# Performance work log

Measured on AMD Instinct MI355X. Metric: run time of the kernel, lower is better.

The kernel has to match this reference:

```python
import jax, jax.numpy as jnp
import numpy as np

D = 1024   # visual_dim
N = 64     # num_phrases(1) * topN(64)
DEG = 16   # edges per subject row (incl. one guaranteed via a permutation)
E = N * DEG
T = 2      # cfg.MODEL.RELATION.VISUAL_GRAPH_PASSING_TIME


def _graph():
    rng = np.random.default_rng(0)
    perm = rng.permutation(N)
    mask = np.zeros((N, N), bool)
    for i in range(N):
        mask[i, perm[i]] = True  # permutation guarantees every column is covered
        pool = np.delete(np.arange(N), perm[i])
        mask[i, rng.choice(pool, DEG - 1, replace=False)] = True
    hdim, wdim = np.nonzero(mask)  # row-major, exactly E entries
    conn = np.full((N, N), -1, np.int32)
    conn[hdim, wdim] = np.arange(hdim.shape[0])
    edge_idx = hdim * N + wdim  # original: hdim*topN + wdim (topN == N since num_phrases == 1)
    return conn, edge_idx.astype(np.int32)


def setup_inputs():
    conn, edge_idx = _graph()
    key = jax.random.key(0)
    ks = jax.random.split(key, 16)
    p = lambda k, shp: jax.random.normal(k, shp, jnp.float32) * 0.02
    return {
        'visual_feat': jax.random.normal(ks[0], (N, D), jnp.float32),
        'rel_visual_feat': jax.random.normal(ks[1], (E, D), jnp.float32),
        'conn_map': jnp.asarray(conn),
        'topN_boxes_ids': jnp.arange(N, dtype=jnp.int32)[None, :],  # only shape is used
        'edge_idx': jnp.asarray(edge_idx),
        'W_sub': p(ks[2], (D, D)),
        'W_obj': p(ks[3], (D, D)),
        'W_r2s': p(ks[4], (D, D)),
        'W_r2o': p(ks[5], (D, D)),
        'W_joint': p(ks[6], (D, 4 * D)),
        'W_ctx': p(ks[7], (D, 3 * D)),
        'W_rel_update': p(ks[8], (D, 3 * D)),
        'W_rel_joint': p(ks[9], (D, 4 * D)),
        'W_rel_ctx': p(ks[10], (D, 2 * D)),
        'W_node': p(ks[11], (D, 2 * D)),
        'b_node': jnp.zeros((D,), jnp.float32),
        'W_factor': p(ks[12], (D, 2 * D)),
    }


def _forward(visual_feat, rel_visual_feat, conn_map, edge_idx,
             W_sub, W_obj, W_r2s, W_r2o, W_joint, W_ctx, W_rel_update,
             W_rel_joint, W_rel_ctx, W_node, b_node, W_factor):
    n, d = visual_feat.shape
    scale = jnp.asarray(d, visual_feat.dtype) ** 0.5
    connected = conn_map >= 0
    # scatter edge features into the dense [N, N, D] grid
    rel_temp = (jnp.zeros((n * n, d), visual_feat.dtype)
                .at[edge_idx].set(rel_visual_feat)
                .reshape(n, n, d))
    rel_ctx = rel_temp
    vctx = visual_feat
    for _ in range(T):
        # joint node embedding  [N, D]
        vj = jnp.concatenate([visual_feat, vctx, visual_feat * vctx, vctx - visual_feat], 1) @ W_joint.T
        # joint edge embedding  [N, N, D] (1x1 conv == per-position linear)
        rj = jnp.einsum('ijd,od->ijo',
                        jnp.concatenate([rel_temp, rel_ctx, rel_temp * rel_ctx, rel_temp - rel_ctx], 2),
                        W_rel_joint)
        # node -> edge: cat(sub_tile, obj_tile, rj) @ W_rel_update, done without tiling
        Ws, Wo, Wr = W_rel_update[:, :d], W_rel_update[:, d:2 * d], W_rel_update[:, 2 * d:]
        rel_j = (vj @ Ws.T)[:, None, :] + (vj @ Wo.T)[None, :, :] + jnp.einsum('ijd,od->ijo', rj, Wr)
        # edge -> node attention scores (elementwise product of 1x1-conv outputs, summed over channels)
        s_sbj = jnp.einsum('id,ijd->ij', vj @ W_sub.T, jnp.einsum('ijd,od->ijo', rel_j, W_r2s)) / scale
        s_obj = jnp.einsum('jd,ijd->ij', vj @ W_obj.T, jnp.einsum('ijd,od->ijo', rel_j, W_r2o)) / scale
        w_sbj = jax.nn.softmax(jnp.where(connected, s_sbj, -jnp.inf), axis=1)
        w_obj = jax.nn.softmax(jnp.where(connected, s_obj, -jnp.inf), axis=0)
        ctx = jnp.concatenate([jnp.einsum('ijd,ij->id', rel_j, w_sbj),
                               jnp.einsum('ijd,ij->jd', rel_j, w_obj)], 1)
        vctx = jnp.concatenate([vctx, ctx], 1) @ W_ctx.T
        rel_ctx = jnp.einsum('ijd,od->ijo', jnp.concatenate([rel_ctx, rel_j], 2), W_rel_ctx)
    # gather back the valid edges and produce outputs
    rel_out = jnp.concatenate([rel_visual_feat, rel_ctx.reshape(-1, d)[edge_idx]], 1) @ W_factor.T
    v_out = jnp.concatenate([visual_feat, vctx], 1) @ W_node.T + b_node
    deg = connected.sum(1) + connected.sum(0)
    v_out = jnp.where((deg == 0)[:, None], visual_feat, v_out)  # isolated nodes pass through
    return rel_out, v_out


def reference(visual_feat, rel_visual_feat, conn_map, topN_boxes_ids, edge_idx,
              W_sub, W_obj, W_r2s, W_r2o, W_joint, W_ctx, W_rel_update,
              W_rel_joint, W_rel_ctx, W_node, b_node, W_factor):
    del topN_boxes_ids  # only its shape is used in the original
    return _forward(visual_feat, rel_visual_feat, conn_map, edge_idx,
                    W_sub, W_obj, W_r2s, W_r2o, W_joint, W_ctx, W_rel_update,
                    W_rel_joint, W_rel_ctx, W_node, b_node, W_factor)
```

## Files before the change

kernel.cpp:

```cpp
#include <hip/hip_runtime.h>

static constexpr int kN = 64;
static constexpr int kD = 1024;
static constexpr int kE = 1024;
static constexpr int kT = 2;

typedef short  bf16x8 __attribute__((ext_vector_type(8)));
typedef float  f32x4  __attribute__((ext_vector_type(4)));
typedef unsigned short us8 __attribute__((ext_vector_type(8)));
typedef unsigned short us4 __attribute__((ext_vector_type(4)));

__device__ __forceinline__ unsigned short f2b(float f) {
    unsigned int u = __builtin_bit_cast(unsigned int, f);
    u += 0x7FFFu + ((u >> 16) & 1u);
    return (unsigned short)(u >> 16);
}
__device__ __forceinline__ float b2f(unsigned short u) {
    unsigned int x = ((unsigned int)u) << 16;
    return __builtin_bit_cast(float, x);
}
__device__ __forceinline__ bf16x8 cvt8(float4 a, float4 b) {
    us8 o;
    o[0] = f2b(a.x); o[1] = f2b(a.y); o[2] = f2b(a.z); o[3] = f2b(a.w);
    o[4] = f2b(b.x); o[5] = f2b(b.y); o[6] = f2b(b.z); o[7] = f2b(b.w);
    return __builtin_bit_cast(bf16x8, o);
}

struct ASrc { const unsigned short* s0; const unsigned short* s1; const unsigned short* s2; int mode; };

__device__ __forceinline__ bf16x8 loadA8(const ASrc& s, int row, int kg) {
    const int seg = kg >> 10, k = kg & 1023;
    const size_t ro = (size_t)row * 1024 + k;
    if (s.mode == 1) {
        const unsigned short* p = (seg == 0) ? s.s0 : (seg == 1 ? s.s1 : s.s2);
        return *(const bf16x8*)(p + ro);
    }
    const bf16x8 a = *(const bf16x8*)(s.s0 + ro);
    if (seg == 0) return a;
    const bf16x8 b = *(const bf16x8*)(s.s1 + ro);
    const us8 ua = __builtin_bit_cast(us8, a), ub = __builtin_bit_cast(us8, b);
    us8 o;
#pragma unroll
    for (int q = 0; q < 8; ++q) o[q] = f2b(b2f(ua[q]) * b2f(ub[q]));
    return __builtin_bit_cast(bf16x8, o);
}

struct GJob { ASrc a; const unsigned short* W; int ldw; void* P; int M; int K; int KS; int pbf; };
struct GJobs { GJob j[5]; int t0[6]; int nj; };

__global__ __launch_bounds__(256)
void k_gemm(GJobs G)
{
    __shared__ unsigned short lds[16896];
    const int flat = blockIdx.x;
    int ji = 0;
    while (ji + 1 < G.nj && flat >= G.t0[ji + 1]) ++ji;
    const GJob J = G.j[ji];
    const int local = flat - G.t0[ji];
    const int tid = threadIdx.x, lane = tid & 63, wid = tid >> 6;
    const int l15 = lane & 15, l4 = lane >> 4;
    const int sr = tid >> 3, sc8 = tid & 7;
    const int wc8 = (sc8 ^ (sr & 7)) * 8;

    if (J.M >= 128) {
        const int rowTiles = J.M >> 7;
        const int rt = local % rowTiles;
        const int rest = local / rowTiles;
        const int ct = rest & 7, z = rest >> 3;
        const int rowBase = rt * 128, colBase = ct * 128;
        const int kchunk = J.K / J.KS, kbeg = z * kchunk, kend = kbeg + kchunk;
        const int wr = wid >> 1, wc = wid & 1;

        f32x4 acc[4][4] = {};
        bf16x8 ra[4], rb[4];
        auto stage = [&](int kt) {
#pragma unroll
            for (int h = 0; h < 4; ++h) {
                ra[h] = loadA8(J.a, rowBase + sr + 32 * h, kt + sc8 * 8);
                rb[h] = *(const bf16x8*)(J.W + (size_t)(colBase + sr + 32 * h) * J.ldw + kt + sc8 * 8);
            }
        };

        stage(kbeg);
        for (int kt = kbeg; kt < kend; kt += 64) {
            __syncthreads();
#pragma unroll
            for (int h = 0; h < 4; ++h) {
                *(bf16x8*)&lds[(sr + 32 * h) * 64 + wc8] = ra[h];
                *(bf16x8*)&lds[8192 + (sr + 32 * h) * 64 + wc8] = rb[h];
            }
            __syncthreads();
            if (kt + 64 < kend) stage(kt + 64);
#pragma unroll
            for (int kk = 0; kk < 2; ++kk) {
                bf16x8 af[4], bv[4];
#pragma unroll
                for (int m = 0; m < 4; ++m) {
                    const int ar = wr * 64 + m * 16 + l15;
                    af[m] = *(const bf16x8*)&lds[ar * 64 + (((kk << 2) | l4) ^ (ar & 7)) * 8];
                }
#pragma unroll
                for (int n = 0; n < 4; ++n) {
                    const int br = wc * 64 + n * 16 + l15;
                    bv[n] = *(const bf16x8*)&lds[8192 + br * 64 + (((kk << 2) | l4) ^ (br & 7)) * 8];
                }
#pragma unroll
                for (int m = 0; m < 4; ++m)
#pragma unroll
                    for (int n = 0; n < 4; ++n)
                        acc[m][n] = __builtin_amdgcn_mfma_f32_16x16x32_bf16(af[m], bv[n], acc[m][n], 0, 0, 0);
            }
        }

        __syncthreads();
#pragma unroll
        for (int m = 0; m < 4; ++m)
#pragma unroll
            for (int n = 0; n < 4; ++n)
#pragma unroll
                for (int r = 0; r < 4; ++r)
                    lds[(wr * 64 + m * 16 + l4 * 4 + r) * 132 + wc * 64 + n * 16 + l15] =
                        f2b(acc[m][n][r]);
        __syncthreads();
        unsigned short* Pb = (unsigned short*)J.P + (size_t)z * J.M * 1024;
#pragma unroll
        for (int c = tid; c < 2048; c += 256) {
            const int row = c >> 4, ch = c & 15;
            *(bf16x8*)(Pb + (size_t)(rowBase + row) * 1024 + colBase + ch * 8) =
                *(const bf16x8*)&lds[row * 132 + ch * 8];
        }
    } else {
        const int ct = local & 7, z = local >> 3;
        const int colBase = ct * 128;
        const int kchunk = J.K / J.KS, kbeg = z * kchunk, kend = kbeg + kchunk;
        const int wr = wid >> 1, wc = wid & 1;

        bf16x8 ra[2], rb[4];
        auto stage = [&](int kt) {
#pragma unroll
            for (int h = 0; h < 2; ++h)
                ra[h] = loadA8(J.a, sr + 32 * h, kt + sc8 * 8);
#pragma unroll
            for (int h = 0; h < 4; ++h)
                rb[h] = *(const bf16x8*)(J.W + (size_t)(colBase + sr + 32 * h) * J.ldw + kt + sc8 * 8);
        };

        f32x4 acc[2][4] = {};
        stage(kbeg);
        for (int kt = kbeg; kt < kend; kt += 64) {
            __syncthreads();
#pragma unroll
            for (int h = 0; h < 2; ++h)
                *(bf16x8*)&lds[(sr + 32 * h) * 64 + wc8] = ra[h];
#pragma unroll
            for (int h = 0; h < 4; ++h)
                *(bf16x8*)&lds[4096 + (sr + 32 * h) * 64 + wc8] = rb[h];
            __syncthreads();
            if (kt + 64 < kend) stage(kt + 64);
#pragma unroll
            for (int kk = 0; kk < 2; ++kk) {
                const int c8 = kk * 4 + l4;
                bf16x8 af[2], bv[4];
#pragma unroll
                for (int m = 0; m < 2; ++m) {
                    const int ar = wr * 32 + m * 16 + l15;
                    af[m] = *(const bf16x8*)&lds[ar * 64 + (c8 ^ (ar & 7)) * 8];
                }
#pragma unroll
                for (int n = 0; n < 4; ++n) {
                    const int br = wc * 64 + n * 16 + l15;
                    bv[n] = *(const bf16x8*)&lds[4096 + br * 64 + (c8 ^ (br & 7)) * 8];
                }
#pragma unroll
                for (int m = 0; m < 2; ++m)
#pragma unroll
                    for (int n = 0; n < 4; ++n)
                        acc[m][n] = __builtin_amdgcn_mfma_f32_16x16x32_bf16(af[m], bv[n], acc[m][n], 0, 0, 0);
            }
        }
        float* base = (float*)J.P + (size_t)z * J.M * 1024;
#pragma unroll
        for (int m = 0; m < 2; ++m) {
            const int row = wr * 32 + m * 16 + l4 * 4;
#pragma unroll
            for (int n = 0; n < 4; ++n) {
                const int col = colBase + wc * 64 + n * 16 + l15;
#pragma unroll
                for (int r = 0; r < 4; ++r)
                    base[(size_t)(row + r) * 1024 + col] = acc[m][n][r];
            }
        }
    }
}

struct RJob { const void* P; int MO8; int KS; int pbf; float* Cf; unsigned short* Cb;
              const unsigned short* addb; const float* bias; int gather; };
struct RJobs { RJob j[6]; int t0[7]; int nj; const int* eidx; const float* gP; int gKS; };

__global__ void k_reduce(RJobs R)
{
    const int flat = blockIdx.x;
    int ji = 0;
    while (ji + 1 < R.nj && flat >= R.t0[ji + 1]) ++ji;
    const RJob J = R.j[ji];
    const int i8 = (flat - R.t0[ji]) * 256 + threadIdx.x;
    if (i8 >= J.MO8) return;
    float s[8] = {0.f, 0.f, 0.f, 0.f, 0.f, 0.f, 0.f, 0.f};
    if (J.pbf) {
        const unsigned short* P = (const unsigned short*)J.P;
        for (int z = 0; z < J.KS; ++z) {
            const us8 v = *(const us8*)(P + (size_t)z * J.MO8 * 8 + (size_t)i8 * 8);
#pragma unroll
            for (int q = 0; q < 8; ++q) s[q] += b2f(v[q]);
        }
    } else {
        const float* P = (const float*)J.P;
        for (int z = 0; z < J.KS; ++z) {
            const float* p = P + (size_t)z * J.MO8 * 8 + (size_t)i8 * 8;
            const float4 v0 = *(const float4*)p;
            const float4 v1 = *(const float4*)(p + 4);
            s[0] += v0.x; s[1] += v0.y; s[2] += v0.z; s[3] += v0.w;
            s[4] += v1.x; s[5] += v1.y; s[6] += v1.z; s[7] += v1.w;
        }
    }
    if (J.addb) {
        const us8 v = *(const us8*)(J.addb + (size_t)i8 * 8);
#pragma unroll
        for (int q = 0; q < 8; ++q) s[q] += b2f(v[q]);
    }
    if (J.gather) {
        const int e = i8 >> 7, c8 = i8 & 127;
        const int idx = R.eidx[e];
        const float* as_ = R.gP + (size_t)(idx >> 6) * 1024 + c8 * 8;
        const float* ao_ = R.gP + 131072 + (size_t)(idx & 63) * 1024 + c8 * 8;
        for (int z = 0; z < R.gKS; ++z) {
#pragma unroll
            for (int q = 0; q < 8; ++q)
                s[q] += as_[(size_t)z * 65536 + q] + ao_[(size_t)z * 65536 + q];
        }
    }
    if (J.bias) {
        const int c8 = i8 & 127;
#pragma unroll
        for (int q = 0; q < 8; ++q) s[q] += J.bias[c8 * 8 + q];
    }
    if (J.Cf) {
        *(float4*)(J.Cf + (size_t)i8 * 8)     = make_float4(s[0], s[1], s[2], s[3]);
        *(float4*)(J.Cf + (size_t)i8 * 8 + 4) = make_float4(s[4], s[5], s[6], s[7]);
    }
    if (J.Cb) {
        us8 o;
#pragma unroll
        for (int q = 0; q < 8; ++q) o[q] = f2b(s[q]);
        *(us8*)(J.Cb + (size_t)i8 * 8) = o;
    }
}

struct ConvBatch { const float* s[7]; unsigned short* d[7]; int beg8[7]; int total8; };
__global__ void k_f2b_batch(ConvBatch cb)
{
    int i = blockIdx.x * blockDim.x + threadIdx.x;
    if (i >= cb.total8) return;
    int k = 0;
    while (k < 6 && i >= cb.beg8[k + 1]) ++k;
    const int j = i - cb.beg8[k];
    const float4 v0 = reinterpret_cast<const float4*>(cb.s[k])[2 * j];
    const float4 v1 = reinterpret_cast<const float4*>(cb.s[k])[2 * j + 1];
    const bf16x8 o = cvt8(v0, v1);
    *(bf16x8*)(cb.d[k] + (size_t)j * 8) = o;
}

struct T4 { const float* s[4]; unsigned short* d[4]; };
__global__ __launch_bounds__(256)
void k_transpose(T4 t4)
{
    __shared__ float tile[64][65];
    const float* __restrict__ src = t4.s[blockIdx.z];
    unsigned short* __restrict__ dst = t4.d[blockIdx.z];
    const int bx = blockIdx.x * 64, by = blockIdx.y * 64;
    const int c = threadIdx.x & 63, r0 = threadIdx.x >> 6;
#pragma unroll
    for (int h = 0; h < 16; ++h) {
        const int r = r0 * 16 + h;
        tile[r][c] = src[(size_t)(by + r) * 1024 + bx + c];
    }
    __syncthreads();
#pragma unroll
    for (int h = 0; h < 16; ++h) {
        const int kk = r0 * 16 + h;
        dst[(size_t)(bx + kk) * 1024 + by + c] = f2b(tile[c][kk]);
    }
}

__global__ __launch_bounds__(256)
void k_buildW(const float* __restrict__ Wrel, const float* __restrict__ Wjnt,
              unsigned short* __restrict__ WrtRel, unsigned short* __restrict__ WeffRel,
              unsigned short* __restrict__ UrtVj, unsigned short* __restrict__ UeffVj)
{
    const int idx = blockIdx.x * 256 + threadIdx.x;
    const int o = idx >> 8, j = (idx & 255) * 4;
    const float* W = blockIdx.z ? Wjnt : Wrel;
    const float sgn = blockIdx.z ? -1.f : 1.f;
    unsigned short* rt = blockIdx.z ? UrtVj : WrtRel;
    unsigned short* ef = blockIdx.z ? UeffVj : WeffRel;
    const float4 w1 = *(const float4*)(W + (size_t)o * 4096 + j);
    const float4 w2 = *(const float4*)(W + (size_t)o * 4096 + 1024 + j);
    const float4 w3 = *(const float4*)(W + (size_t)o * 4096 + 2048 + j);
    const float4 w4 = *(const float4*)(W + (size_t)o * 4096 + 3072 + j);
    us4 t;
    t.x = f2b(w1.x + sgn * w4.x); t.y = f2b(w1.y + sgn * w4.y);
    t.z = f2b(w1.z + sgn * w4.z); t.w = f2b(w1.w + sgn * w4.w);
    *(us4*)(rt + (size_t)o * 1024 + j) = t;
    t.x = f2b(w2.x - sgn * w4.x); t.y = f2b(w2.y - sgn * w4.y);
    t.z = f2b(w2.z - sgn * w4.z); t.w = f2b(w2.w - sgn * w4.w);
    *(us4*)(ef + (size_t)o * 2048 + j) = t;
    t.x = f2b(w3.x); t.y = f2b(w3.y); t.z = f2b(w3.z); t.w = f2b(w3.w);
    *(us4*)(ef + (size_t)o * 2048 + 1024 + j) = t;
}

__global__ __launch_bounds__(256)
void k_sctx(const float* __restrict__ relj, const float* __restrict__ qws,
            const float* __restrict__ qwo, const int* __restrict__ conn,
            unsigned short* __restrict__ ctx1b, unsigned short* __restrict__ ctx2b)
{
    const int bid = blockIdx.x, t = threadIdx.x;
    const float4* relj4 = reinterpret_cast<const float4*>(relj);
    __shared__ float sl[64];
    __shared__ int el[64];
    float4 acc = make_float4(0.f, 0.f, 0.f, 0.f);

    if (bid < 64) {
        const int i = bid;
        {
            const int g = t >> 4, l = t & 15;
            const size_t e4 = (size_t)(i * 16 + g) * 256;
            const float4* q4 = reinterpret_cast<const float4*>(qws) + (size_t)i * 256;
            float v = 0.f;
#pragma unroll
            for (int q = 0; q < 16; ++q) {
                const float4 r = relj4[e4 + l + q * 16];
                const float4 a = q4[l + q * 16];
                v += a.x * r.x + a.y * r.y + a.z * r.z + a.w * r.w;
            }
            v += __shfl_xor(v, 1, 16);
            v += __shfl_xor(v, 2, 16);
            v += __shfl_xor(v, 4, 16);
            v += __shfl_xor(v, 8, 16);
            if (l == 0) sl[g] = v * 0.03125f;
        }
        __syncthreads();
        float sv[16];
        float m = -1e30f;
#pragma unroll
        for (int q = 0; q < 16; ++q) { sv[q] = sl[q]; m = fmaxf(m, sv[q]); }
        float sum = 0.f;
#pragma unroll
        for (int q = 0; q < 16; ++q) { sv[q] = expf(sv[q] - m); sum += sv[q]; }
        const float inv = 1.f / sum;
#pragma unroll
        for (int q = 0; q < 16; ++q) {
            const float w = sv[q] * inv;
            const float4 v = relj4[(size_t)(i * 16 + q) * 256 + t];
            acc.x += w * v.x; acc.y += w * v.y; acc.z += w * v.z; acc.w += w * v.w;
        }
        us4 o; o.x = f2b(acc.x); o.y = f2b(acc.y); o.z = f2b(acc.z); o.w = f2b(acc.w);
        *(us4*)(ctx1b + (size_t)i * 1024 + t * 4) = o;
    } else {
        const int j = bid - 64;
        {
            const int i = t >> 2, sub = t & 3;
            const int e = conn[i * kN + j];
            if (sub == 0) el[i] = e;
            float v = 0.f;
            if (e >= 0) {
                const size_t e4 = (size_t)e * 256;
                const float4* q4 = reinterpret_cast<const float4*>(qwo) + (size_t)j * 256;
#pragma unroll
                for (int q = 0; q < 64; ++q) {
                    const float4 r = relj4[e4 + sub + q * 4];
                    const float4 a = q4[sub + q * 4];
                    v += a.x * r.x + a.y * r.y + a.z * r.z + a.w * r.w;
                }
            }
            v += __shfl_xor(v, 1, 4);
            v += __shfl_xor(v, 2, 4);
            if (sub == 0) sl[i] = (e >= 0) ? v * 0.03125f : -1e30f;
        }
        __syncthreads();
        float m = -1e30f;
        for (int i = 0; i < 64; ++i) m = fmaxf(m, sl[i]);
        float sum = 0.f;
        float ex[64];
        for (int i = 0; i < 64; ++i) {
            ex[i] = (el[i] >= 0) ? expf(sl[i] - m) : 0.f;
            sum += ex[i];
        }
        const float inv = 1.f / sum;
        for (int i = 0; i < 64; ++i) {
            const int e = el[i];
            if (e >= 0) {
                const float w = ex[i] * inv;
                const float4 v = relj4[(size_t)e * 256 + t];
                acc.x += w * v.x; acc.y += w * v.y; acc.z += w * v.z; acc.w += w * v.w;
            }
        }
        us4 o; o.x = f2b(acc.x); o.y = f2b(acc.y); o.z = f2b(acc.z); o.w = f2b(acc.w);
        *(us4*)(ctx2b + (size_t)j * 1024 + t * 4) = o;
    }
}

extern "C" void kernel_launch(void* const* d_in, const int* in_sizes, int n_in,
                              void* d_out, int out_size, void* d_ws, size_t ws_size,
                              hipStream_t stream)
{
    const float* visual   = (const float*)d_in[0];
    const float* relvis   = (const float*)d_in[1];
    const int*   conn     = (const int*)d_in[2];
    const int*   edge_idx = (const int*)d_in[4];
    const float* W_sub    = (const float*)d_in[5];
    const float* W_obj    = (const float*)d_in[6];
    const float* W_r2s    = (const float*)d_in[7];
    const float* W_r2o    = (const float*)d_in[8];
    const float* W_joint  = (const float*)d_in[9];
    const float* W_ctx    = (const float*)d_in[10];
    const float* W_relu   = (const float*)d_in[11];
    const float* W_relj   = (const float*)d_in[12];
    const float* W_relc   = (const float*)d_in[13];
    const float* W_node   = (const float*)d_in[14];
    const float* b_node   = (const float*)d_in[15];
    const float* W_factor = (const float*)d_in[16];
    (void)in_sizes; (void)n_in; (void)out_size; (void)ws_size;

    float* ws = (float*)d_ws;
    size_t off = 0;
    auto allocF = [&](size_t n) { float* p = ws + off; off += n; return p; };
    auto allocU = [&](size_t n) { return (unsigned short*)allocF((n + 1) / 2); };

    float* partF = allocF((size_t)1024 * 1024);
    unsigned short* partB = allocU((size_t)16 * 1024 * 1024);
    float* asqw  = allocF((size_t)4 * 64 * 1024);
    float* relj  = allocF((size_t)kE * kD);
    unsigned short* relvis_b = allocU((size_t)kE * kD);
    unsigned short* visual_b = allocU((size_t)kN * kD);
    unsigned short* vj_b   = allocU((size_t)kN * kD);
    unsigned short* rj_b   = allocU((size_t)kE * kD);
    unsigned short* relj_b = allocU((size_t)kE * kD);
    unsigned short* rc_bA  = allocU((size_t)kE * kD);
    unsigned short* rc_bB  = allocU((size_t)kE * kD);
    unsigned short* vctx_bA = allocU((size_t)kN * kD);
    unsigned short* vctx_bB = allocU((size_t)kN * kD);
    unsigned short* ctx1_b = allocU((size_t)kN * kD);
    unsigned short* ctx2_b = allocU((size_t)kN * kD);
    unsigned short* R0_b = allocU((size_t)kE * kD);
    unsigned short* G0_b = allocU((size_t)kN * kD);
    unsigned short* Wb_ctx    = allocU((size_t)kD * 3 * kD);
    unsigned short* Wb_relu   = allocU((size_t)kD * 3 * kD);
    unsigned short* Wb_relc   = allocU((size_t)kD * 2 * kD);
    unsigned short* Wb_node   = allocU((size_t)kD * 2 * kD);
    unsigned short* Wb_factor = allocU((size_t)kD * 2 * kD);
    unsigned short* WsubT = allocU((size_t)kD * kD);
    unsigned short* WobjT = allocU((size_t)kD * kD);
    unsigned short* Wr2sT = allocU((size_t)kD * kD);
    unsigned short* Wr2oT = allocU((size_t)kD * kD);
    unsigned short* Wc_s  = allocU((size_t)kD * kD);
    unsigned short* Wc_o  = allocU((size_t)kD * kD);
    unsigned short* WrtRel  = allocU((size_t)kD * kD);
    unsigned short* WeffRel = allocU((size_t)kD * 2 * kD);
    unsigned short* UrtVj   = allocU((size_t)kD * kD);
    unsigned short* UeffVj  = allocU((size_t)kD * 2 * kD);

    auto seg1 = [](const unsigned short* a) {
        ASrc s; s.s0 = a; s.s1 = nullptr; s.s2 = nullptr; s.mode = 1; return s;
    };
    auto seg2 = [](const unsigned short* a, const unsigned short* b) {
        ASrc s; s.s0 = a; s.s1 = b; s.s2 = nullptr; s.mode = 1; return s;
    };
    auto seg3 = [](const unsigned short* a, const unsigned short* b, const unsigned short* c) {
        ASrc s; s.s0 = a; s.s1 = b; s.s2 = c; s.mode = 1; return s;
    };
    auto prodA = [](const unsigned short* c, const unsigned short* x) {
        ASrc s; s.s0 = c; s.s1 = x; s.s2 = nullptr; s.mode = 2; return s;
    };

    GJobs G; RJobs R;
    int gn = 0, gt = 0, rn = 0, rtt = 0;
    auto gAdd = [&](ASrc a, const unsigned short* W, int ldw, void* P, int M, int K, int KS, int pbf) {
        G.j[gn].a = a; G.j[gn].W = W; G.j[gn].ldw = ldw; G.j[gn].P = P;
        G.j[gn].M = M; G.j[gn].K = K; G.j[gn].KS = KS; G.j[gn].pbf = pbf;
        G.t0[gn] = gt;
        gt += (M >= 128) ? KS * (M >> 7) * 8 : KS * 8;
        ++gn;
    };
    auto gLaunch = [&]() {
        G.nj = gn; G.t0[gn] = gt;
        hipLaunchKernelGGL(k_gemm, dim3(gt), dim3(256), 0, stream, G);
        gn = 0; gt = 0;
    };
    auto rAdd = [&](const void* P, int MO8, int KS, int pbf, float* Cf, unsigned short* Cb,
                    const unsigned short* addb, const float* bias, int gather) {
        R.j[rn].P = P; R.j[rn].MO8 = MO8; R.j[rn].KS = KS; R.j[rn].pbf = pbf;
        R.j[rn].Cf = Cf; R.j[rn].Cb = Cb; R.j[rn].addb = addb; R.j[rn].bias = bias;
        R.j[rn].gather = gather;
        R.t0[rn] = rtt; rtt += (MO8 + 255) / 256; ++rn;
    };
    auto rLaunch = [&](const int* eidx, const float* gP, int gKS) {
        R.nj = rn; R.t0[rn] = rtt; R.eidx = eidx; R.gP = gP; R.gKS = gKS;
        hipLaunchKernelGGL(k_reduce, dim3(rtt), dim3(256), 0, stream, R);
        rn = 0; rtt = 0;
    };

    {
        ConvBatch cb;
        const float* srcs[7] = {W_ctx, W_relu, W_relc, W_node, W_factor, relvis, visual};
        unsigned short* dsts[7] = {Wb_ctx, Wb_relu, Wb_relc, Wb_node, Wb_factor, relvis_b, visual_b};
        const int nel[7] = {3 * 1024 * 1024, 3 * 1024 * 1024, 2 * 1024 * 1024,
                            2 * 1024 * 1024, 2 * 1024 * 1024, 1024 * 1024, 64 * 1024};
        int cum = 0;
        for (int k = 0; k < 7; ++k) { cb.s[k] = srcs[k]; cb.d[k] = dsts[k]; cb.beg8[k] = cum; cum += nel[k] / 8; }
        cb.total8 = cum;
        hipLaunchKernelGGL(k_f2b_batch, dim3((cum + 255) / 256), dim3(256), 0, stream, cb);
    }
    {
        T4 t4;
        t4.s[0] = W_sub; t4.d[0] = WsubT;
        t4.s[1] = W_obj; t4.d[1] = WobjT;
        t4.s[2] = W_r2s; t4.d[2] = Wr2sT;
        t4.s[3] = W_r2o; t4.d[3] = Wr2oT;
        hipLaunchKernelGGL(k_transpose, dim3(16, 16, 4), dim3(256), 0, stream, t4);
    }
    hipLaunchKernelGGL(k_buildW, dim3(1024, 1, 2), dim3(256), 0, stream,
                       W_relj, W_joint, WrtRel, WeffRel, UrtVj, UeffVj);

    const size_t PB1 = (size_t)4 * 1024 * 1024;
    gAdd(seg1(Wr2sT), WsubT, 1024, partB, 1024, 1024, 4, 1);
    gAdd(seg1(Wr2oT), WobjT, 1024, partB + PB1, 1024, 1024, 4, 1);
    gAdd(seg1(relvis_b), WrtRel, 1024, partB + 2 * PB1, 1024, 1024, 4, 1);
    gAdd(seg1(visual_b), UrtVj, 1024, partF, 64, 1024, 4, 0);
    gLaunch();
    rAdd(partB, 131072, 4, 1, nullptr, Wc_s, nullptr, nullptr, 0);
    rAdd(partB + PB1, 131072, 4, 1, nullptr, Wc_o, nullptr, nullptr, 0);
    rAdd(partB + 2 * PB1, 131072, 4, 1, nullptr, R0_b, nullptr, nullptr, 0);
    rAdd(partF, 8192, 4, 0, nullptr, G0_b, nullptr, nullptr, 0);
    rLaunch(nullptr, nullptr, 0);

    for (int t = 0; t < kT; ++t) {
        const unsigned short* vcur  = (t == 0) ? visual_b : vctx_bA;
        unsigned short*       vnext = (t == 0) ? vctx_bA : vctx_bB;
        const unsigned short* rccur = (t == 0) ? relvis_b : rc_bA;
        unsigned short*       rcnext = (t == 0) ? rc_bA : rc_bB;

        gAdd(prodA(vcur, visual_b), UeffVj, 2048, partF, 64, 2048, 8, 0);
        gAdd(prodA(rccur, relvis_b), WeffRel, 2048, partB, 1024, 2048, 8, 1);
        gLaunch();
        rAdd(partF, 8192, 8, 0, nullptr, vj_b, G0_b, nullptr, 0);
        rAdd(partB, 131072, 8, 1, nullptr, rj_b, R0_b, nullptr, 0);
        rLaunch(nullptr, nullptr, 0);

        gAdd(seg1(vj_b), Wb_relu,        3072, partF,          64, 1024, 2, 0);
        gAdd(seg1(vj_b), Wb_relu + 1024, 3072, partF + 131072, 64, 1024, 2, 0);
        gAdd(seg1(vj_b), Wc_s,           1024, partF + 262144, 64, 1024, 2, 0);
        gAdd(seg1(vj_b), Wc_o,           1024, partF + 393216, 64, 1024, 2, 0);
        gAdd(seg1(rj_b), Wb_relu + 2048, 3072, partB,        1024, 1024, 4, 1);
        gLaunch();
        rAdd(partF,          8192, 2, 0, asqw,          nullptr, nullptr, nullptr, 0);
        rAdd(partF + 131072, 8192, 2, 0, asqw + 65536,  nullptr, nullptr, nullptr, 0);
        rAdd(partF + 262144, 8192, 2, 0, asqw + 131072, nullptr, nullptr, nullptr, 0);
        rAdd(partF + 393216, 8192, 2, 0, asqw + 196608, nullptr, nullptr, nullptr, 0);
        rAdd(partB, 131072, 4, 1, relj, relj_b, nullptr, nullptr, 1);
        rLaunch(edge_idx, partF, 2);

        hipLaunchKernelGGL(k_sctx, dim3(128), dim3(256), 0, stream,
                           relj, asqw + 131072, asqw + 196608, conn, ctx1_b, ctx2_b);

        gAdd(seg3(vcur, ctx1_b, ctx2_b), Wb_ctx, 3072, partF, 64, 3072, 8, 0);
        gAdd(seg2(rccur, relj_b), Wb_relc, 2048, partB, 1024, 2048, 8, 1);
        gLaunch();
        rAdd(partF, 8192, 8, 0, nullptr, vnext, nullptr, nullptr, 0);
        rAdd(partB, 131072, 8, 1, nullptr, rcnext, nullptr, nullptr, 0);
        rLaunch(nullptr, nullptr, 0);
    }

    float* rel_out = (float*)d_out;
    float* v_out   = (float*)d_out + (size_t)kE * kD;
    gAdd(seg2(relvis_b, rc_bB), Wb_factor, 2048, partB, 1024, 2048, 4, 1);
    gAdd(seg2(visual_b, vctx_bB), Wb_node, 2048, partF, 64, 2048, 8, 0);
    gLaunch();
    rAdd(partB, 131072, 4, 1, rel_out, nullptr, nullptr, nullptr, 0);
    rAdd(partF, 8192, 8, 0, v_out, nullptr, nullptr, b_node, 0);
    rLaunch(nullptr, nullptr, 0);
}
```

Measured before the change: 230.0 us.

## Fuse split-K reduction into GEMM via last-block atomic counter epilogue

```diff
diff --git a/kernel.cpp b/kernel.cpp
--- a/kernel.cpp
+++ b/kernel.cpp
@@ -45,143 +45,102 @@
     return __builtin_bit_cast(bf16x8, o);
 }
 
-struct GJob { ASrc a; const unsigned short* W; int ldw; void* P; int M; int K; int KS; int pbf; };
-struct GJobs { GJob j[5]; int t0[6]; int nj; };
+struct GEpi { float* Cf; unsigned short* Cb; const unsigned short* addb;
+              const float* bias; int tail; int cbase; };
+struct GJob { ASrc a; const unsigned short* W; int ldw; void* P; int M; int K; int KS; int pbf;
+              GEpi e; };
+struct GJobs { GJob j[6]; int t0[7]; int nj; int* cnt; };
 
 __global__ __launch_bounds__(256)
 void k_gemm(GJobs G)
 {
-    __shared__ unsigned short lds[16896];
+    __shared__ unsigned short lds[12288];
+    __shared__ int lastFlag;
     const int flat = blockIdx.x;
     int ji = 0;
     while (ji + 1 < G.nj && flat >= G.t0[ji + 1]) ++ji;
     const GJob J = G.j[ji];
     const int local = flat - G.t0[ji];
+    const int rowTiles = J.M >> 6;
+    const int rt = local & (rowTiles - 1);
+    const int rest = local / rowTiles;
+    const int ct = rest & 7, z = rest >> 3;
+    const int rowBase = rt * 64, colBase = ct * 128;
+    const int kchunk = J.K / J.KS, kbeg = z * kchunk, kend = kbeg + kchunk;
+
     const int tid = threadIdx.x, lane = tid & 63, wid = tid >> 6;
     const int l15 = lane & 15, l4 = lane >> 4;
     const int sr = tid >> 3, sc8 = tid & 7;
     const int wc8 = (sc8 ^ (sr & 7)) * 8;
-
-    if (J.M >= 128) {
-        const int rowTiles = J.M >> 7;
-        const int rt = local % rowTiles;
-        const int rest = local / rowTiles;
-        const int ct = rest & 7, z = rest >> 3;
-        const int rowBase = rt * 128, colBase = ct * 128;
-        const int kchunk = J.K / J.KS, kbeg = z * kchunk, kend = kbeg + kchunk;
-        const int wr = wid >> 1, wc = wid & 1;
-
-        f32x4 acc[4][4] = {};
-        bf16x8 ra[4], rb[4];
-        auto stage = [&](int kt) {
-#pragma unroll
-            for (int h = 0; h < 4; ++h) {
-                ra[h] = loadA8(J.a, rowBase + sr + 32 * h, kt + sc8 * 8);
-                rb[h] = *(const bf16x8*)(J.W + (size_t)(colBase + sr + 32 * h) * J.ldw + kt + sc8 * 8);
-            }
-        };
-
-        stage(kbeg);
-        for (int kt = kbeg; kt < kend; kt += 64) {
-            __syncthreads();
-#pragma unroll
-            for (int h = 0; h < 4; ++h) {
-                *(bf16x8*)&lds[(sr + 32 * h) * 64 + wc8] = ra[h];
-                *(bf16x8*)&lds[8192 + (sr + 32 * h) * 64 + wc8] = rb[h];
-            }
-            __syncthreads();
-            if (kt + 64 < kend) stage(kt + 64);
-#pragma unroll
-            for (int kk = 0; kk < 2; ++kk) {
-                bf16x8 af[4], bv[4];
-#pragma unroll
-                for (int m = 0; m < 4; ++m) {
-                    const int ar = wr * 64 + m * 16 + l15;
-                    af[m] = *(const bf16x8*)&lds[ar * 64 + (((kk << 2) | l4) ^ (ar & 7)) * 8];
-                }
-#pragma unroll
-                for (int n = 0; n < 4; ++n) {
-                    const int br = wc * 64 + n * 16 + l15;
-                    bv[n] = *(const bf16x8*)&lds[8192 + br * 64 + (((kk << 2) | l4) ^ (br & 7)) * 8];
-                }
-#pragma unroll
-                for (int m = 0; m < 4; ++m)
-#pragma unroll
-                    for (int n = 0; n < 4; ++n)
-                        acc[m][n] = __builtin_amdgcn_mfma_f32_16x16x32_bf16(af[m], bv[n], acc[m][n], 0, 0, 0);
-            }
-        }
-
+    const int wr = wid >> 1, wc = wid & 1;
+
+    bf16x8 ra[2], rb[4];
+    auto stage = [&](int kt) {
+#pragma unroll
+        for (int h = 0; h < 2; ++h)
+            ra[h] = loadA8(J.a, rowBase + sr + 32 * h, kt + sc8 * 8);
+#pragma unroll
+        for (int h = 0; h < 4; ++h)
+            rb[h] = *(const bf16x8*)(J.W + (size_t)(colBase + sr + 32 * h) * J.ldw + kt + sc8 * 8);
+    };
+
+    f32x4 acc[2][4] = {};
+    stage(kbeg);
+    for (int kt = kbeg; kt < kend; kt += 64) {
         __syncthreads();
 #pragma unroll
-        for (int m = 0; m < 4; ++m)
+        for (int h = 0; h < 2; ++h)
+            *(bf16x8*)&lds[(sr + 32 * h) * 64 + wc8] = ra[h];
+#pragma unroll
+        for (int h = 0; h < 4; ++h)
+            *(bf16x8*)&lds[4096 + (sr + 32 * h) * 64 + wc8] = rb[h];
+        __syncthreads();
+        if (kt + 64 < kend) stage(kt + 64);
+#pragma unroll
+        for (int kk = 0; kk < 2; ++kk) {
+            const int c8 = kk * 4 + l4;
+            bf16x8 af[2], bv[4];
+#pragma unroll
+            for (int m = 0; m < 2; ++m) {
+                const int ar = wr * 32 + m * 16 + l15;
+                af[m] = *(const bf16x8*)&lds[ar * 64 + (c8 ^ (ar & 7)) * 8];
+            }
+#pragma unroll
+            for (int n = 0; n < 4; ++n) {
+                const int br = wc * 64 + n * 16 + l15;
+                bv[n] = *(const bf16x8*)&lds[4096 + br * 64 + (c8 ^ (br & 7)) * 8];
+            }
+#pragma unroll
+            for (int m = 0; m < 2; ++m)
+#pragma unroll
+                for (int n = 0; n < 4; ++n)
+                    acc[m][n] = __builtin_amdgcn_mfma_f32_16x16x32_bf16(af[m], bv[n], acc[m][n], 0, 0, 0);
+        }
+    }
+
+    if (J.pbf) {
+        __syncthreads();
+#pragma unroll
+        for (int m = 0; m < 2; ++m)
 #pragma unroll
             for (int n = 0; n < 4; ++n)
 #pragma unroll
                 for (int r = 0; r < 4; ++r)
-                    lds[(wr * 64 + m * 16 + l4 * 4 + r) * 132 + wc * 64 + n * 16 + l15] =
+                    lds[(wr * 32 + m * 16 + l4 * 4 + r) * 132 + wc * 64 + n * 16 + l15] =
                         f2b(acc[m][n][r]);
         __syncthreads();
         unsigned short* Pb = (unsigned short*)J.P + (size_t)z * J.M * 1024;
 #pragma unroll
-        for (int c = tid; c < 2048; c += 256) {
+        for (int c = tid; c < 1024; c += 256) {
             const int row = c >> 4, ch = c & 15;
             *(bf16x8*)(Pb + (size_t)(rowBase + row) * 1024 + colBase + ch * 8) =
                 *(const bf16x8*)&lds[row * 132 + ch * 8];
         }
     } else {
-        const int ct = local & 7, z = local >> 3;
-        const int colBase = ct * 128;
-        const int kchunk = J.K / J.KS, kbeg = z * kchunk, kend = kbeg + kchunk;
-        const int wr = wid >> 1, wc = wid & 1;
-
-        bf16x8 ra[2], rb[4];
-        auto stage = [&](int kt) {
-#pragma unroll
-            for (int h = 0; h < 2; ++h)
-                ra[h] = loadA8(J.a, sr + 32 * h, kt + sc8 * 8);
-#pragma unroll
-            for (int h = 0; h < 4; ++h)
-                rb[h] = *(const bf16x8*)(J.W + (size_t)(colBase + sr + 32 * h) * J.ldw + kt + sc8 * 8);
-        };
-
-        f32x4 acc[2][4] = {};
-        stage(kbeg);
-        for (int kt = kbeg; kt < kend; kt += 64) {
-            __syncthreads();
-#pragma unroll
-            for (int h = 0; h < 2; ++h)
-                *(bf16x8*)&lds[(sr + 32 * h) * 64 + wc8] = ra[h];
-#pragma unroll
-            for (int h = 0; h < 4; ++h)
-                *(bf16x8*)&lds[4096 + (sr + 32 * h) * 64 + wc8] = rb[h];
-            __syncthreads();
-            if (kt + 64 < kend) stage(kt + 64);
-#pragma unroll
-            for (int kk = 0; kk < 2; ++kk) {
-                const int c8 = kk * 4 + l4;
-                bf16x8 af[2], bv[4];
-#pragma unroll
-                for (int m = 0; m < 2; ++m) {
-                    const int ar = wr * 32 + m * 16 + l15;
-                    af[m] = *(const bf16x8*)&lds[ar * 64 + (c8 ^ (ar & 7)) * 8];
-                }
-#pragma unroll
-                for (int n = 0; n < 4; ++n) {
-                    const int br = wc * 64 + n * 16 + l15;
-                    bv[n] = *(const bf16x8*)&lds[4096 + br * 64 + (c8 ^ (br & 7)) * 8];
-                }
-#pragma unroll
-                for (int m = 0; m < 2; ++m)
-#pragma unroll
-                    for (int n = 0; n < 4; ++n)
-                        acc[m][n] = __builtin_amdgcn_mfma_f32_16x16x32_bf16(af[m], bv[n], acc[m][n], 0, 0, 0);
-            }
-        }
         float* base = (float*)J.P + (size_t)z * J.M * 1024;
 #pragma unroll
         for (int m = 0; m < 2; ++m) {
-            const int row = wr * 32 + m * 16 + l4 * 4;
+            const int row = rowBase + wr * 32 + m * 16 + l4 * 4;
 #pragma unroll
             for (int n = 0; n < 4; ++n) {
                 const int col = colBase + wc * 64 + n * 16 + l15;
@@ -191,69 +150,87 @@
             }
         }
     }
-}
-
-struct RJob { const void* P; int MO8; int KS; int pbf; float* Cf; unsigned short* Cb;
-              const unsigned short* addb; const float* bias; int gather; };
-struct RJobs { RJob j[6]; int t0[7]; int nj; const int* eidx; const float* gP; int gKS; };
-
-__global__ void k_reduce(RJobs R)
-{
-    const int flat = blockIdx.x;
-    int ji = 0;
-    while (ji + 1 < R.nj && flat >= R.t0[ji + 1]) ++ji;
-    const RJob J = R.j[ji];
-    const int i8 = (flat - R.t0[ji]) * 256 + threadIdx.x;
-    if (i8 >= J.MO8) return;
+
+    if (!J.e.tail) return;
+    __syncthreads();
+    if (tid == 0) {
+        __threadfence();
+        lastFlag = (atomicAdd(&G.cnt[J.e.cbase + rt * 8 + ct], 1) == J.KS - 1);
+    }
+    __syncthreads();
+    if (!lastFlag) return;
+    __threadfence();
+
+    const int rr = tid >> 2, c0 = (tid & 3) * 32;
+    const int grow = rowBase + rr;
+#pragma unroll
+    for (int g = 0; g < 4; ++g) {
+        const int col = colBase + c0 + g * 8;
+        const size_t oidx = (size_t)grow * 1024 + col;
+        float s[8] = {0.f, 0.f, 0.f, 0.f, 0.f, 0.f, 0.f, 0.f};
+        if (J.pbf) {
+            const unsigned short* Pb = (const unsigned short*)J.P;
+            for (int zz = 0; zz < J.KS; ++zz) {
+                const us8 v = *(const us8*)(Pb + (size_t)zz * J.M * 1024 + oidx);
+#pragma unroll
+                for (int q = 0; q < 8; ++q) s[q] += b2f(v[q]);
+            }
+        } else {
+            const float* Pf = (const float*)J.P;
+            for (int zz = 0; zz < J.KS; ++zz) {
+                const float* p = Pf + (size_t)zz * J.M * 1024 + oidx;
+                const float4 v0 = *(const float4*)p;
+                const float4 v1 = *(const float4*)(p + 4);
+                s[0] += v0.x; s[1] += v0.y; s[2] += v0.z; s[3] += v0.w;
+                s[4] += v1.x; s[5] += v1.y; s[6] += v1.z; s[7] += v1.w;
+            }
+        }
+        if (J.e.addb) {
+            const us8 v = *(const us8*)(J.e.addb + oidx);
+#pragma unroll
+            for (int q = 0; q < 8; ++q) s[q] += b2f(v[q]);
+        }
+        if (J.e.bias) {
+#pragma unroll
+            for (int q = 0; q < 8; ++q) s[q] += J.e.bias[col + q];
+        }
+        if (J.e.Cf) {
+            *(float4*)(J.e.Cf + oidx)     = make_float4(s[0], s[1], s[2], s[3]);
+            *(float4*)(J.e.Cf + oidx + 4) = make_float4(s[4], s[5], s[6], s[7]);
+        }
+        if (J.e.Cb) {
+            us8 o;
+#pragma unroll
+            for (int q = 0; q < 8; ++q) o[q] = f2b(s[q]);
+            *(us8*)(J.e.Cb + oidx) = o;
+        }
+    }
+}
+
+__global__ void k_relj(const unsigned short* __restrict__ P, int KS,
+                       const float* __restrict__ a_s, const float* __restrict__ a_o,
+                       const int* __restrict__ eidx,
+                       float* __restrict__ Cf, unsigned short* __restrict__ Cb)
+{
+    const int i8 = blockIdx.x * 256 + threadIdx.x;
     float s[8] = {0.f, 0.f, 0.f, 0.f, 0.f, 0.f, 0.f, 0.f};
-    if (J.pbf) {
-        const unsigned short* P = (const unsigned short*)J.P;
-        for (int z = 0; z < J.KS; ++z) {
-            const us8 v = *(const us8*)(P + (size_t)z * J.MO8 * 8 + (size_t)i8 * 8);
-#pragma unroll
-            for (int q = 0; q < 8; ++q) s[q] += b2f(v[q]);
-        }
-    } else {
-        const float* P = (const float*)J.P;
-        for (int z = 0; z < J.KS; ++z) {
-            const float* p = P + (size_t)z * J.MO8 * 8 + (size_t)i8 * 8;
-            const float4 v0 = *(const float4*)p;
-            const float4 v1 = *(const float4*)(p + 4);
-            s[0] += v0.x; s[1] += v0.y; s[2] += v0.z; s[3] += v0.w;
-            s[4] += v1.x; s[5] += v1.y; s[6] += v1.z; s[7] += v1.w;
-        }
-    }
-    if (J.addb) {
-        const us8 v = *(const us8*)(J.addb + (size_t)i8 * 8);
+    for (int z = 0; z < KS; ++z) {
+        const us8 v = *(const us8*)(P + (size_t)z * 1048576 + (size_t)i8 * 8);
 #pragma unroll
         for (int q = 0; q < 8; ++q) s[q] += b2f(v[q]);
     }
-    if (J.gather) {
-        const int e = i8 >> 7, c8 = i8 & 127;
-        const int idx = R.eidx[e];
-        const float* as_ = R.gP + (size_t)(idx >> 6) * 1024 + c8 * 8;
-        const float* ao_ = R.gP + 131072 + (size_t)(idx & 63) * 1024 + c8 * 8;
-        for (int z = 0; z < R.gKS; ++z) {
-#pragma unroll
-            for (int q = 0; q < 8; ++q)
-                s[q] += as_[(size_t)z * 65536 + q] + ao_[(size_t)z * 65536 + q];
-        }
-    }
-    if (J.bias) {
-        const int c8 = i8 & 127;
-#pragma unroll
-        for (int q = 0; q < 8; ++q) s[q] += J.bias[c8 * 8 + q];
-    }
-    if (J.Cf) {
-        *(float4*)(J.Cf + (size_t)i8 * 8)     = make_float4(s[0], s[1], s[2], s[3]);
-        *(float4*)(J.Cf + (size_t)i8 * 8 + 4) = make_float4(s[4], s[5], s[6], s[7]);
-    }
-    if (J.Cb) {
-        us8 o;
-#pragma unroll
-        for (int q = 0; q < 8; ++q) o[q] = f2b(s[q]);
-        *(us8*)(J.Cb + (size_t)i8 * 8) = o;
-    }
+    const int e = i8 >> 7, c8 = i8 & 127;
+    const int idx = eidx[e];
+    const float* as_ = a_s + (size_t)(idx >> 6) * 1024 + c8 * 8;
+    const float* ao_ = a_o + (size_t)(idx & 63) * 1024 + c8 * 8;
+#pragma unroll
+    for (int q = 0; q < 8; ++q) s[q] += as_[q] + ao_[q];
+    *(float4*)(Cf + (size_t)i8 * 8)     = make_float4(s[0], s[1], s[2], s[3]);
+    *(float4*)(Cf + (size_t)i8 * 8 + 4) = make_float4(s[4], s[5], s[6], s[7]);
+    us8 o;
+#pragma unroll
+    for (int q = 0; q < 8; ++q) o[q] = f2b(s[q]);
+    *(us8*)(Cb + (size_t)i8 * 8) = o;
 }
 
 struct ConvBatch { const float* s[7]; unsigned short* d[7]; int beg8[7]; int total8; };
@@ -431,8 +408,9 @@
     const float* W_factor = (const float*)d_in[16];
     (void)in_sizes; (void)n_in; (void)out_size; (void)ws_size;
 
+    int* cnt = (int*)d_ws;
     float* ws = (float*)d_ws;
-    size_t off = 0;
+    size_t off = 2048;
     auto allocF = [&](size_t n) { float* p = ws + off; off += n; return p; };
     auto allocU = [&](size_t n) { return (unsigned short*)allocF((n + 1) / 2); };
 
@@ -481,33 +459,33 @@
     auto prodA = [](const unsigned short* c, const unsigned short* x) {
         ASrc s; s.s0 = c; s.s1 = x; s.s2 = nullptr; s.mode = 2; return s;
     };
-
-    GJobs G; RJobs R;
-    int gn = 0, gt = 0, rn = 0, rtt = 0;
-    auto gAdd = [&](ASrc a, const unsigned short* W, int ldw, void* P, int M, int K, int KS, int pbf) {
+    auto epi = [](float* Cf, unsigned short* Cb, const unsigned short* addb,
+                  const float* bias) {
+        GEpi e; e.Cf = Cf; e.Cb = Cb; e.addb = addb; e.bias = bias; e.tail = 1; e.cbase = 0;
+        return e;
+    };
+    auto noepi = []() {
+        GEpi e; e.Cf = nullptr; e.Cb = nullptr; e.addb = nullptr; e.bias = nullptr;
+        e.tail = 0; e.cbase = 0; return e;
+    };
+
+    GJobs G;
+    G.cnt = cnt;
+    int gn = 0, gt = 0, cOff = 0;
+    auto gAdd = [&](ASrc a, const unsigned short* W, int ldw, void* P, int M, int K, int KS,
+                    int pbf, GEpi e) {
+        if (e.tail) { e.cbase = cOff; cOff += (M >> 6) * 8; }
         G.j[gn].a = a; G.j[gn].W = W; G.j[gn].ldw = ldw; G.j[gn].P = P;
-        G.j[gn].M = M; G.j[gn].K = K; G.j[gn].KS = KS; G.j[gn].pbf = pbf;
-        G.t0[gn] = gt;
-        gt += (M >= 128) ? KS * (M >> 7) * 8 : KS * 8;
-        ++gn;
+        G.j[gn].M = M; G.j[gn].K = K; G.j[gn].KS = KS; G.j[gn].pbf = pbf; G.j[gn].e = e;
+        G.t0[gn] = gt; gt += KS * (M >> 6) * 8; ++gn;
     };
     auto gLaunch = [&]() {
         G.nj = gn; G.t0[gn] = gt;
         hipLaunchKernelGGL(k_gemm, dim3(gt), dim3(256), 0, stream, G);
         gn = 0; gt = 0;
     };
-    auto rAdd = [&](const void* P, int MO8, int KS, int pbf, float* Cf, unsigned short* Cb,
-                    const unsigned short* addb, const float* bias, int gather) {
-        R.j[rn].P = P; R.j[rn].MO8 = MO8; R.j[rn].KS = KS; R.j[rn].pbf = pbf;
-        R.j[rn].Cf = Cf; R.j[rn].Cb = Cb; R.j[rn].addb = addb; R.j[rn].bias = bias;
-        R.j[rn].gather = gather;
-        R.t0[rn] = rtt; rtt += (MO8 + 255) / 256; ++rn;
-    };
-    auto rLaunch = [&](const int* eidx, const float* gP, int gKS) {
-        R.nj = rn; R.t0[rn] = rtt; R.eidx = eidx; R.gP = gP; R.gKS = gKS;
-        hipLaunchKernelGGL(k_reduce, dim3(rtt), dim3(256), 0, stream, R);
-        rn = 0; rtt = 0;
-    };
+
+    hipMemsetAsync(cnt, 0, 2048 * sizeof(int), stream);
 
     {
         ConvBatch cb;
@@ -531,17 +509,12 @@
     hipLaunchKernelGGL(k_buildW, dim3(1024, 1, 2), dim3(256), 0, stream,
                        W_relj, W_joint, WrtRel, WeffRel, UrtVj, UeffVj);
 
-    const size_t PB1 = (size_t)4 * 1024 * 1024;
-    gAdd(seg1(Wr2sT), WsubT, 1024, partB, 1024, 1024, 4, 1);
-    gAdd(seg1(Wr2oT), WobjT, 1024, partB + PB1, 1024, 1024, 4, 1);
-    gAdd(seg1(relvis_b), WrtRel, 1024, partB + 2 * PB1, 1024, 1024, 4, 1);
-    gAdd(seg1(visual_b), UrtVj, 1024, partF, 64, 1024, 4, 0);
+    const size_t PB4 = (size_t)4 * 1024 * 1024;
+    gAdd(seg1(Wr2sT), WsubT, 1024, partB,           1024, 1024, 4, 1, epi(nullptr, Wc_s, nullptr, nullptr));
+    gAdd(seg1(Wr2oT), WobjT, 1024, partB + PB4,     1024, 1024, 4, 1, epi(nullptr, Wc_o, nullptr, nullptr));
+    gAdd(seg1(relvis_b), WrtRel, 1024, partB + 2 * PB4, 1024, 1024, 4, 1, epi(nullptr, R0_b, nullptr, nullptr));
+    gAdd(seg1(visual_b), UrtVj, 1024, partF, 64, 1024, 4, 0, epi(nullptr, G0_b, nullptr, nullptr));
     gLaunch();
-    rAdd(partB, 131072, 4, 1, nullptr, Wc_s, nullptr, nullptr, 0);
-    rAdd(partB + PB1, 131072, 4, 1, nullptr, Wc_o, nullptr, nullptr, 0);
-    rAdd(partB + 2 * PB1, 131072, 4, 1, nullptr, R0_b, nullptr, nullptr, 0);
-    rAdd(partF, 8192, 4, 0, nullptr, G0_b, nullptr, nullptr, 0);
-    rLaunch(nullptr, nullptr, 0);
 
     for (int t = 0; t < kT; ++t) {
         const unsigned short* vcur  = (t == 0) ? visual_b : vctx_bA;
@@ -549,43 +522,41 @@
         const unsigned short* rccur = (t == 0) ? relvis_b : rc_bA;
         unsigned short*       rcnext = (t == 0) ? rc_bA : rc_bB;
 
-        gAdd(prodA(vcur, visual_b), UeffVj, 2048, partF, 64, 2048, 8, 0);
-        gAdd(prodA(rccur, relvis_b), WeffRel, 2048, partB, 1024, 2048, 8, 1);
+        gAdd(prodA(vcur, visual_b), UeffVj, 2048, partF, 64, 2048, 8, 0,
+             epi(nullptr, vj_b, G0_b, nullptr));
+        gAdd(prodA(rccur, relvis_b), WeffRel, 2048, partB, 1024, 2048, 8, 1,
+             epi(nullptr, rj_b, R0_b, nullptr));
         gLaunch();
-        rAdd(partF, 8192, 8, 0, nullptr, vj_b, G0_b, nullptr, 0);
-        rAdd(partB, 131072, 8, 1, nullptr, rj_b, R0_b, nullptr, 0);
-        rLaunch(nullptr, nullptr, 0);
-
-        gAdd(seg1(vj_b), Wb_relu,        3072, partF,          64, 1024, 2, 0);
-        gAdd(seg1(vj_b), Wb_relu + 1024, 3072, partF + 131072, 64, 1024, 2, 0);
-        gAdd(seg1(vj_b), Wc_s,           1024, partF + 262144, 64, 1024, 2, 0);
-        gAdd(seg1(vj_b), Wc_o,           1024, partF + 393216, 64, 1024, 2, 0);
-        gAdd(seg1(rj_b), Wb_relu + 2048, 3072, partB,        1024, 1024, 4, 1);
+
+        gAdd(seg1(vj_b), Wb_relu,        3072, partF,          64, 1024, 2, 0,
+             epi(asqw,          nullptr, nullptr, nullptr));
+        gAdd(seg1(vj_b), Wb_relu + 1024, 3072, partF + 131072, 64, 1024, 2, 0,
+             epi(asqw + 65536,  nullptr, nullptr, nullptr));
+        gAdd(seg1(vj_b), Wc_s,           1024, partF + 262144, 64, 1024, 2, 0,
+             epi(asqw + 131072, nullptr, nullptr, nullptr));
+        gAdd(seg1(vj_b), Wc_o,           1024, partF + 393216, 64, 1024, 2, 0,
+             epi(asqw + 196608, nullptr, nullptr, nullptr));
+        gAdd(seg1(rj_b), Wb_relu + 2048, 3072, partB, 1024, 1024, 4, 1, noepi());
         gLaunch();
-        rAdd(partF,          8192, 2, 0, asqw,          nullptr, nullptr, nullptr, 0);
-        rAdd(partF + 131072, 8192, 2, 0, asqw + 65536,  nullptr, nullptr, nullptr, 0);
-        rAdd(partF + 262144, 8192, 2, 0, asqw + 131072, nullptr, nullptr, nullptr, 0);
-        rAdd(partF + 393216, 8192, 2, 0, asqw + 196608, nullptr, nullptr, nullptr, 0);
-        rAdd(partB, 131072, 4, 1, relj, relj_b, nullptr, nullptr, 1);
-        rLaunch(edge_idx, partF, 2);
+
+        hipLaunchKernelGGL(k_relj, dim3(512), dim3(256), 0, stream,
+                           partB, 4, asqw, asqw + 65536, edge_idx, relj, relj_b);
 
         hipLaunchKernelGGL(k_sctx, dim3(128), dim3(256), 0, stream,
                            relj, asqw + 131072, asqw + 196608, conn, ctx1_b, ctx2_b);
 
-        gAdd(seg3(vcur, ctx1_b, ctx2_b), Wb_ctx, 3072, partF, 64, 3072, 8, 0);
-        gAdd(seg2(rccur, relj_b), Wb_relc, 2048, partB, 1024, 2048, 8, 1);
+        gAdd(seg3(vcur, ctx1_b, ctx2_b), Wb_ctx, 3072, partF, 64, 3072, 8, 0,
+             epi(nullptr, vnext, nullptr, nullptr));
+        gAdd(seg2(rccur, relj_b), Wb_relc, 2048, partB, 1024, 2048, 8, 1,
+             epi(nullptr, rcnext, nullptr, nullptr));
         gLaunch();
-        rAdd(partF, 8192, 8, 0, nullptr, vnext, nullptr, nullptr, 0);
-        rAdd(partB, 131072, 8, 1, nullptr, rcnext, nullptr, nullptr, 0);
-        rLaunch(nullptr, nullptr, 0);
     }
 
     float* rel_out = (float*)d_out;
     float* v_out   = (float*)d_out + (size_t)kE * kD;
-    gAdd(seg2(relvis_b, rc_bB), Wb_factor, 2048, partB, 1024, 2048, 4, 1);
-    gAdd(seg2(visual_b, vctx_bB), Wb_node, 2048, partF, 64, 2048, 8, 0);
+    gAdd(seg2(relvis_b, rc_bB), Wb_factor, 2048, partB, 1024, 2048, 4, 1,
+         epi(rel_out, nullptr, nullptr, nullptr));
+    gAdd(seg2(visual_b, vctx_bB), Wb_node, 2048, partF, 64, 2048, 8, 0,
+         epi(v_out, nullptr, nullptr, b_node));
     gLaunch();
-    rAdd(partB, 131072, 4, 1, rel_out, nullptr, nullptr, nullptr, 0);
-    rAdd(partF, 8192, 8, 0, v_out, nullptr, nullptr, b_node, 0);
-    rLaunch(nullptr, nullptr, 0);
-}
+}
```

Result: slower. 606.3 us (+163.6%).
